# Kernel tuning notes

Measured on AMD Instinct MI355X. Metric: run time of the kernel, lower is better.

Reference implementation:

```python
import math
import jax, jax.numpy as jnp
import numpy as np

H_CYCLES, L_CYCLES = 3, 2
STD = 0.02


def setup_inputs() -> dict:
    key = jax.random.key(0)
    ks = jax.random.split(key, 11)
    D, nh, mult, V, T, B = 512, 8, 64, 8192, 512, 4
    N = mult * D // nh
    def nrm(k, shape):
        return jax.random.normal(k, shape, jnp.float32) * STD
    return {
        "idx": jax.random.randint(ks[0], (B, T), 0, V),
        "embed_w": nrm(ks[1], (V, D)),
        "h_enc": nrm(ks[2], (nh, D, N)),
        "h_enc_v": nrm(ks[3], (nh, D, N)),
        "h_dec": nrm(ks[4], (nh * N, D)),
        "l_enc": nrm(ks[5], (nh, D, N)),
        "l_enc_v": nrm(ks[6], (nh, D, N)),
        "l_dec": nrm(ks[7], (nh * N, D)),
        "lm_head": nrm(ks[8], (D, V)),
        "h_init": nrm(ks[9], (D,)),
        "l_init": nrm(ks[10], (D,)),
    }


def _ln(x, eps=1e-5):
    # LayerNorm without affine params (elementwise_affine=False)
    m = jnp.mean(x, axis=-1, keepdims=True)
    v = jnp.var(x, axis=-1, keepdims=True)
    return (x - m) * jax.lax.rsqrt(v + eps)


def _rope_tables(T, N):
    # freqs with even-quantized exponent, angles wrapped mod 1 then scaled by 2*pi
    q = jnp.floor(jnp.arange(N, dtype=jnp.float32) / 2.0) * 2.0
    freqs = 1.0 / jnp.power(2.0 ** 16, q / N) / (2.0 * math.pi)
    phases = jnp.arange(T, dtype=jnp.float32)[:, None] * freqs[None, :]
    ang = (phases % 1.0) * (2.0 * math.pi)
    return jnp.cos(ang), jnp.sin(ang)  # each (T, N)


def _rope(v, cos, sin):
    # v: (B, nh, T, N); interleaved rotation as in torch stack/view trick
    v_rot = jnp.stack((-v[..., 1::2], v[..., ::2]), axis=-1).reshape(v.shape)
    return v * cos + v_rot * sin


def _attn(x_sparse, Vmat, cos, sin):
    # x_sparse: (B, nh, T, N); Vmat: (B, T, D)
    N = x_sparse.shape[-1]
    T = x_sparse.shape[-2]
    QR = _rope(x_sparse, cos, sin)
    scores = jnp.einsum('bhtn,bhsn->bhts', QR, QR) * (N ** -0.5)
    mask = jnp.tril(jnp.ones((T, T), dtype=bool), k=-1)  # strict lower triangle
    scores = jnp.where(mask, scores, 0.0)
    return jnp.einsum('bhts,bsd->bhtd', scores, Vmat)  # (B, nh, T, D)


def _block(x, inj, enc, enc_v, dec, cos, sin):
    # x, inj: (B, 1, T, D)
    B, _, T, D = x.shape
    nh, _, N = enc.shape
    xi = _ln(x + inj)[:, 0]  # (B, T, D)
    x_sparse = jax.nn.relu(jnp.einsum('btd,hdn->bhtn', xi, enc))
    yKV = _ln(_attn(x_sparse, xi, cos, sin))  # (B, nh, T, D)
    y_sparse = jax.nn.relu(jnp.einsum('bhtd,hdn->bhtn', yKV, enc_v))
    xy = (x_sparse * y_sparse).transpose(0, 2, 1, 3).reshape(B, 1, T, nh * N)
    y = _ln(xy @ dec)  # (B, 1, T, D)
    return _ln(x + y)


def reference(idx, embed_w, h_enc, h_enc_v, h_dec, l_enc, l_enc_v, l_dec,
              lm_head, h_init, l_init):
    B, T = idx.shape
    D = embed_w.shape[1]
    N = l_enc.shape[-1]
    cos, sin = _rope_tables(T, N)
    inp = _ln(embed_w[idx])[:, None]  # (B, 1, T, D)
    z_H = jnp.broadcast_to(h_init, (B, 1, T, D))
    z_L = jnp.broadcast_to(l_init, (B, 1, T, D))
    for h in range(H_CYCLES):
        for l in range(L_CYCLES):
            if not (h == H_CYCLES - 1 and l == L_CYCLES - 1):
                z_L = _block(z_L, z_H + inp, l_enc, l_enc_v, l_dec, cos, sin)
        if h < H_CYCLES - 1:
            z_H = _block(z_H, z_L, h_enc, h_enc_v, h_dec, cos, sin)
    z_L = _block(z_L, z_H + inp, l_enc, l_enc_v, l_dec, cos, sin)
    z_H = _block(z_H, z_L, h_enc, h_enc_v, h_dec, cos, sin)
    logits = z_H[:, 0] @ lm_head  # (B, T, vocab)
    return logits
```

## Files before the change

### kernel.cpp

```cpp
#include <hip/hip_runtime.h>

typedef _Float16 f16;
typedef __attribute__((ext_vector_type(8))) _Float16 f16x8;
typedef __attribute__((ext_vector_type(4))) float f32x4;
typedef __attribute__((ext_vector_type(4))) int i32x4;

#define D_  512
#define NH_ 8
#define NS_ 4096
#define TT_ 512
#define BB_ 4
#define VV_ 8192
#define HN_ 32768
#define BT_ 2048


__device__ __forceinline__ void gl16(const void* g, void* l) {
  __builtin_amdgcn_global_load_lds((const __attribute__((address_space(1))) void*)g,
                                   (__attribute__((address_space(3))) void*)l, 16, 0, 0);
}

__device__ __forceinline__ void gemm_core(const f16* __restrict__ A, const f16* __restrict__ B,
    int lda, int ldb, int nk, char* As, char* Bs, f32x4 acc[4][4]) {
  int tid = threadIdx.x;
  int l = tid & 63, wid = tid >> 6;
  int wm = wid >> 1, wn = wid & 1;
  int row0 = tid >> 3, g0 = tid & 7;
  for (int kt = 0; kt < nk; ++kt) {
    __syncthreads();
#pragma unroll
    for (int it = 0; it < 4; ++it) {
      int row = row0 + 32 * it;
      int gs = g0 ^ (row & 7);
      int wb = (wid * 64 + it * 256) * 16;
      gl16(A + (size_t)row * lda + gs * 8, As + wb);
      gl16(B + (size_t)row * ldb + gs * 8, Bs + wb);
    }
    __syncthreads();
    A += 64; B += 64;
#pragma unroll
    for (int kh = 0; kh < 2; ++kh) {
      f16x8 af[4], bfr[4];
#pragma unroll
      for (int m = 0; m < 4; ++m) {
        int row = wm * 64 + m * 16 + (l & 15);
        af[m] = *(const f16x8*)(As + row * 128 + ((kh * 64 + (l >> 4) * 16) ^ ((row & 7) << 4)));
      }
#pragma unroll
      for (int n = 0; n < 4; ++n) {
        int row = wn * 64 + n * 16 + (l & 15);
        bfr[n] = *(const f16x8*)(Bs + row * 128 + ((kh * 64 + (l >> 4) * 16) ^ ((row & 7) << 4)));
      }
#pragma unroll
      for (int m = 0; m < 4; ++m)
#pragma unroll
        for (int n = 0; n < 4; ++n)
          acc[m][n] = __builtin_amdgcn_mfma_f32_16x16x32_f16(af[m], bfr[n], acc[m][n], 0, 0, 0);
    }
  }
}

__device__ __forceinline__ void gemm_core_w(const f16* __restrict__ A, const f16* __restrict__ B,
    int lda, int ldb, int nk, char* As, char* Bs, f32x4 acc[4][4]) {
  int tid = threadIdx.x;
  int l = tid & 63, wid = tid >> 6;
  int wm = wid >> 2, wn = wid & 3;
  int row0 = tid >> 3, g0 = tid & 7;
  for (int kt = 0; kt < nk; ++kt) {
    __syncthreads();
#pragma unroll
    for (int it = 0; it < 2; ++it) {
      int row = row0 + 64 * it;
      int gs = g0 ^ (row & 7);
      gl16(A + (size_t)row * lda + gs * 8, As + (wid * 64 + it * 512) * 16);
    }
#pragma unroll
    for (int it = 0; it < 4; ++it) {
      int row = row0 + 64 * it;
      int gs = g0 ^ (row & 7);
      gl16(B + (size_t)row * ldb + gs * 8, Bs + (wid * 64 + it * 512) * 16);
    }
    __syncthreads();
    A += 64; B += 64;
#pragma unroll
    for (int kh = 0; kh < 2; ++kh) {
      f16x8 af[4], bfr[4];
#pragma unroll
      for (int m = 0; m < 4; ++m) {
        int row = wm * 64 + m * 16 + (l & 15);
        af[m] = *(const f16x8*)(As + row * 128 + ((kh * 64 + (l >> 4) * 16) ^ ((row & 7) << 4)));
      }
#pragma unroll
      for (int n = 0; n < 4; ++n) {
        int row = wn * 64 + n * 16 + (l & 15);
        bfr[n] = *(const f16x8*)(Bs + row * 128 + ((kh * 64 + (l >> 4) * 16) ^ ((row & 7) << 4)));
      }
#pragma unroll
      for (int m = 0; m < 4; ++m)
#pragma unroll
        for (int n = 0; n < 4; ++n)
          acc[m][n] = __builtin_amdgcn_mfma_f32_16x16x32_f16(af[m], bfr[n], acc[m][n], 0, 0, 0);
    }
  }
}


__global__ __launch_bounds__(512, 4) void k_gemm_xs(
    const f16* __restrict__ xi, const f16* __restrict__ encT,
    const f16* __restrict__ csT, f16* __restrict__ qr) {
  __shared__ char sh[49152];
  int bid = blockIdx.x;
  int h = bid & 7, k = bid >> 3;
  int nt = k >> 4, mt = k & 15;
  const f16* A = xi + (size_t)mt * 128 * D_;
  const f16* B = encT + ((size_t)h * NS_ + nt * 256) * D_;
  f32x4 acc[4][4] = {};
  gemm_core_w(A, B, D_, D_, D_ / 64, sh, sh + 16384, acc);
  int l = threadIdx.x & 63, wid = threadIdx.x >> 6;
  int wm = wid >> 2, wn = wid & 3;
  int r04 = (l >> 4) * 4, c0 = l & 15;
  int b = mt >> 2, tbase = (mt & 3) * 128;
#pragma unroll
  for (int m = 0; m < 4; ++m)
#pragma unroll
    for (int n = 0; n < 4; ++n)
#pragma unroll
      for (int r = 0; r < 4; ++r) {
        int row = wm * 64 + m * 16 + r04 + r;
        int col = wn * 64 + n * 16 + c0;
        int t = tbase + row;
        int nn = nt * 256 + col;
        float xsv = fmaxf(acc[m][n][r], 0.f);
        float prt = __shfl_xor(xsv, 1);
        int ci = 2 * (t * NS_ + nn);
        float c = (float)csT[ci], s = (float)csT[ci + 1];
        float qv = xsv * c + ((nn & 1) ? prt : -prt) * s;
        size_t o = (((size_t)b * NH_ + h) * TT_ + t) * NS_ + nn;
        qr[o] = (f16)qv;
      }
}

__global__ __launch_bounds__(256, 4) void k_gemm_scores(
    const f16* __restrict__ qr, f16* __restrict__ scores) {
  __shared__ i32x4 As4[1024], Bs4[1024];
  int bid = blockIdx.x;
  int swz = (bid & 7) * 40 + (bid >> 3);
  int x = swz % 10, z = swz / 10;
  int mt = (x >= 6) ? 3 : (x >= 3) ? 2 : (x >= 1) ? 1 : 0;
  int nt = x - mt * (mt + 1) / 2;
  const f16* base = qr + (size_t)z * TT_ * NS_;
  const f16* A = base + (size_t)mt * 128 * NS_;
  const f16* B = base + (size_t)nt * 128 * NS_;
  f32x4 acc[4][4] = {};
  gemm_core(A, B, NS_, NS_, NS_ / 64, (char*)As4, (char*)Bs4, acc);
  int l = threadIdx.x & 63, wid = threadIdx.x >> 6;
  int wm = wid >> 1, wn = wid & 1;
  int r04 = (l >> 4) * 4, c0 = l & 15;
  f16* outp = scores + (size_t)z * TT_ * TT_;
#pragma unroll
  for (int m = 0; m < 4; ++m)
#pragma unroll
    for (int n = 0; n < 4; ++n)
#pragma unroll
      for (int r = 0; r < 4; ++r) {
        int t = mt * 128 + wm * 64 + m * 16 + r04 + r;
        int s_ = nt * 128 + wn * 64 + n * 16 + c0;
        float v = (t > s_) ? acc[m][n][r] * 0.015625f : 0.f;
        outp[(size_t)t * TT_ + s_] = (f16)v;
      }
}

__global__ __launch_bounds__(256, 4) void k_gemm_attn(
    const f16* __restrict__ scores, const f16* __restrict__ xiT, f16* __restrict__ attn) {
  __shared__ i32x4 As4[1024], Bs4[1024];
  int bid = blockIdx.x;
  int swz = (bid & 7) * 64 + (bid >> 3);
  int mt = swz & 3, ntd = (swz >> 2) & 3, z = swz >> 4;
  int b = z >> 3;
  const f16* A = scores + (size_t)z * TT_ * TT_ + (size_t)mt * 128 * TT_;
  const f16* B = xiT + (size_t)b * D_ * TT_ + (size_t)ntd * 128 * TT_;
  f32x4 acc[4][4] = {};
  gemm_core(A, B, TT_, TT_, 2 * mt + 2, (char*)As4, (char*)Bs4, acc);
  int l = threadIdx.x & 63, wid = threadIdx.x >> 6;
  int wm = wid >> 1, wn = wid & 1;
  int r04 = (l >> 4) * 4, c0 = l & 15;
#pragma unroll
  for (int m = 0; m < 4; ++m)
#pragma unroll
    for (int n = 0; n < 4; ++n)
#pragma unroll
      for (int r = 0; r < 4; ++r) {
        int t = mt * 128 + wm * 64 + m * 16 + r04 + r;
        int d = ntd * 128 + wn * 64 + n * 16 + c0;
        attn[((size_t)z * TT_ + t) * D_ + d] = (f16)acc[m][n][r];
      }
}

__global__ __launch_bounds__(512, 4) void k_gemm_xy(
    const f16* __restrict__ ykv, const f16* __restrict__ encvT,
    const f16* __restrict__ csT, f16* __restrict__ qrxy) {
  __shared__ char sh[49152];
  int bid = blockIdx.x;
  int h = bid & 7, k = bid >> 3;
  int b = k >> 6, nt = (k >> 2) & 15, mt = k & 3;
  int z = b * NH_ + h;
  const f16* A = ykv + (size_t)z * TT_ * D_ + (size_t)mt * 128 * D_;
  const f16* B = encvT + ((size_t)h * NS_ + nt * 256) * D_;
  f32x4 acc[4][4] = {};
  gemm_core_w(A, B, D_, D_, D_ / 64, sh, sh + 16384, acc);
  int l = threadIdx.x & 63, wid = threadIdx.x >> 6;
  int wm = wid >> 2, wn = wid & 3;
  int r04 = (l >> 4) * 4, c0 = l & 15;
#pragma unroll
  for (int m = 0; m < 4; ++m)
#pragma unroll
    for (int n = 0; n < 4; ++n)
#pragma unroll
      for (int r = 0; r < 4; ++r) {
        int t = mt * 128 + wm * 64 + m * 16 + r04 + r;
        int nn = nt * 256 + wn * 64 + n * 16 + c0;
        float ys = fmaxf(acc[m][n][r], 0.f);
        size_t o = ((size_t)z * TT_ + t) * NS_ + nn;
        float qv = (float)qrxy[o];
        float prt = __shfl_xor(qv, 1);
        int ci = 2 * (t * NS_ + nn);
        float c = (float)csT[ci], s = (float)csT[ci + 1];
        float xsv = (nn & 1) ? (qv * c - prt * s) : (qv * c + prt * s);
        qrxy[o] = (f16)(xsv * ys);
      }
}

__global__ __launch_bounds__(512, 4) void k_gemm_ydec(
    const f16* __restrict__ xy, const f16* __restrict__ decT, f16* __restrict__ ypart) {
  __shared__ char sh[49152];
  int bid = blockIdx.x;
  int kz = bid & 7, k = bid >> 3;
  int mt = k >> 1, nt = k & 1;
  int b = mt >> 2, t0 = (mt & 3) * 128;
  const f16* A = xy + ((size_t)(b * NH_ + kz) * TT_ + t0) * NS_;
  const f16* B = decT + (size_t)nt * 256 * HN_ + (size_t)kz * NS_;
  f32x4 acc[4][4] = {};
  gemm_core_w(A, B, NS_, HN_, NS_ / 64, sh, sh + 16384, acc);
  int l = threadIdx.x & 63, wid = threadIdx.x >> 6;
  int wm = wid >> 2, wn = wid & 3;
  int r04 = (l >> 4) * 4, c0 = l & 15;
  f16* outp = ypart + (size_t)kz * BT_ * D_;
#pragma unroll
  for (int m = 0; m < 4; ++m)
#pragma unroll
    for (int n = 0; n < 4; ++n)
#pragma unroll
      for (int r = 0; r < 4; ++r) {
        int R = mt * 128 + wm * 64 + m * 16 + r04 + r;
        int c = nt * 256 + wn * 64 + n * 16 + c0;
        outp[(size_t)R * D_ + c] = (f16)acc[m][n][r];
      }
}

__global__ __launch_bounds__(512, 4) void k_gemm_logits(
    const f16* __restrict__ zbf, const f16* __restrict__ lmT, float* __restrict__ outp) {
  __shared__ char sh[49152];
  int bid = blockIdx.x;
  int xcd = bid & 7, k = bid >> 3;
  int nt = xcd * 4 + (k >> 4), mt = k & 15;
  const f16* A = zbf + (size_t)mt * 128 * D_;
  const f16* B = lmT + (size_t)nt * 256 * D_;
  f32x4 acc[4][4] = {};
  gemm_core_w(A, B, D_, D_, D_ / 64, sh, sh + 16384, acc);
  int l = threadIdx.x & 63, wid = threadIdx.x >> 6;
  int wm = wid >> 2, wn = wid & 3;
  int r04 = (l >> 4) * 4, c0 = l & 15;
#pragma unroll
  for (int m = 0; m < 4; ++m)
#pragma unroll
    for (int n = 0; n < 4; ++n)
#pragma unroll
      for (int r = 0; r < 4; ++r) {
        int R = mt * 128 + wm * 64 + m * 16 + r04 + r;
        int v = nt * 256 + wn * 64 + n * 16 + c0;
        outp[(size_t)R * VV_ + v] = acc[m][n][r];
      }
}


__device__ __forceinline__ float wave_sum(float v) {
#pragma unroll
  for (int o = 32; o > 0; o >>= 1) v += __shfl_xor(v, o);
  return v;
}

__global__ __launch_bounds__(256) void k_tables(f16* __restrict__ csT) {
  int i = blockIdx.x * 256 + threadIdx.x;
  int t = i >> 12, n = i & (NS_ - 1);
  float q = (float)(n & ~1);
  float freq = exp2f(-16.f * q / 4096.f) * 0.15915494309189535f;
  float ph = (float)t * freq;
  ph -= floorf(ph);
  float ang = ph * 6.283185307179586f;
  csT[2 * i]     = (f16)cosf(ang);
  csT[2 * i + 1] = (f16)sinf(ang);
}

__global__ void k_transpose(const float* __restrict__ in, f16* __restrict__ outp, int R, int C) {
  __shared__ float tile[32][33];
  size_t mo = (size_t)blockIdx.z * R * C;
  in += mo; outp += mo;
  int c0 = blockIdx.x * 32, r0 = blockIdx.y * 32;
#pragma unroll
  for (int i = threadIdx.y; i < 32; i += 8)
    tile[i][threadIdx.x] = in[(size_t)(r0 + i) * C + c0 + threadIdx.x];
  __syncthreads();
#pragma unroll
  for (int i = threadIdx.y; i < 32; i += 8)
    outp[(size_t)(c0 + i) * R + r0 + threadIdx.x] = (f16)tile[threadIdx.x][i];
}

__global__ __launch_bounds__(256) void k_embed_ln(const int* __restrict__ idx,
    const float* __restrict__ emb, f16* __restrict__ inp) {
  int r = blockIdx.x * 4 + (threadIdx.x >> 6);
  int lane = threadIdx.x & 63;
  const float* e = emb + (size_t)idx[r] * D_ + lane * 8;
  f32x4 e0 = *(const f32x4*)e;
  f32x4 e1 = *(const f32x4*)(e + 4);
  float v[8];
#pragma unroll
  for (int i = 0; i < 4; ++i) { v[i] = e0[i]; v[i + 4] = e1[i]; }
  float s = 0.f;
#pragma unroll
  for (int i = 0; i < 8; ++i) s += v[i];
  float mean = wave_sum(s) * (1.f / 512.f);
  float q = 0.f;
#pragma unroll
  for (int i = 0; i < 8; ++i) { v[i] -= mean; q += v[i] * v[i]; }
  float rs = rsqrtf(wave_sum(q) * (1.f / 512.f) + 1e-5f);
  f16x8 ov;
#pragma unroll
  for (int i = 0; i < 8; ++i) ov[i] = (f16)(v[i] * rs);
  *(f16x8*)(inp + (size_t)r * D_ + lane * 8) = ov;
}

__global__ __launch_bounds__(256) void k_init(const float* __restrict__ hi,
    const float* __restrict__ li, f16* __restrict__ zH, f16* __restrict__ zL) {
  size_t i = (size_t)blockIdx.x * 256 + threadIdx.x;
  zH[i] = (f16)hi[i & (D_ - 1)];
  zL[i] = (f16)li[i & (D_ - 1)];
}

__global__ __launch_bounds__(256) void k_ln_xi(const f16* __restrict__ x,
    const f16* __restrict__ a1, const f16* __restrict__ a2,
    f16* __restrict__ xi, f16* __restrict__ xiT) {
  int r = blockIdx.x * 4 + (threadIdx.x >> 6);
  int lane = threadIdx.x & 63;
  size_t o = (size_t)r * D_ + lane * 8;
  f16x8 xv = *(const f16x8*)(x + o);
  f16x8 av = *(const f16x8*)(a1 + o);
  float v[8];
#pragma unroll
  for (int i = 0; i < 8; ++i) v[i] = (float)xv[i] + (float)av[i];
  if (a2) {
    f16x8 bv = *(const f16x8*)(a2 + o);
#pragma unroll
    for (int i = 0; i < 8; ++i) v[i] += (float)bv[i];
  }
  float s = 0.f;
#pragma unroll
  for (int i = 0; i < 8; ++i) s += v[i];
  float mean = wave_sum(s) * (1.f / 512.f);
  float q = 0.f;
#pragma unroll
  for (int i = 0; i < 8; ++i) { v[i] -= mean; q += v[i] * v[i]; }
  float rs = rsqrtf(wave_sum(q) * (1.f / 512.f) + 1e-5f);
  f16x8 ov;
#pragma unroll
  for (int i = 0; i < 8; ++i) ov[i] = (f16)(v[i] * rs);
  *(f16x8*)(xi + o) = ov;
  int b = r >> 9, t = r & (TT_ - 1);
  int d0 = lane * 8;
#pragma unroll
  for (int i = 0; i < 8; ++i)
    xiT[((size_t)b * D_ + d0 + i) * TT_ + t] = ov[i];
}

__global__ __launch_bounds__(256) void k_ln_rows(const f16* __restrict__ in, f16* __restrict__ outp) {
  int r = blockIdx.x * 4 + (threadIdx.x >> 6);
  int lane = threadIdx.x & 63;
  size_t o = (size_t)r * D_ + lane * 8;
  f16x8 xv = *(const f16x8*)(in + o);
  float v[8];
#pragma unroll
  for (int i = 0; i < 8; ++i) v[i] = (float)xv[i];
  float s = 0.f;
#pragma unroll
  for (int i = 0; i < 8; ++i) s += v[i];
  float mean = wave_sum(s) * (1.f / 512.f);
  float q = 0.f;
#pragma unroll
  for (int i = 0; i < 8; ++i) { v[i] -= mean; q += v[i] * v[i]; }
  float rs = rsqrtf(wave_sum(q) * (1.f / 512.f) + 1e-5f);
  f16x8 ov;
#pragma unroll
  for (int i = 0; i < 8; ++i) ov[i] = (f16)(v[i] * rs);
  *(f16x8*)(outp + o) = ov;
}

__global__ __launch_bounds__(256) void k_ln_y_out(const f16* __restrict__ ypart,
    f16* __restrict__ z) {
  int r = blockIdx.x * 4 + (threadIdx.x >> 6);
  int lane = threadIdx.x & 63;
  size_t o = (size_t)r * D_ + lane * 8;
  float v[8] = {};
#pragma unroll
  for (int k = 0; k < 8; ++k) {
    f16x8 p = *(const f16x8*)(ypart + (size_t)k * BT_ * D_ + o);
#pragma unroll
    for (int i = 0; i < 8; ++i) v[i] += (float)p[i];
  }
  float s = 0.f;
#pragma unroll
  for (int i = 0; i < 8; ++i) s += v[i];
  float mean = wave_sum(s) * (1.f / 512.f);
  float q = 0.f;
#pragma unroll
  for (int i = 0; i < 8; ++i) { v[i] -= mean; q += v[i] * v[i]; }
  float rs = rsqrtf(wave_sum(q) * (1.f / 512.f) + 1e-5f);
  f16x8 zv = *(const f16x8*)(z + o);
#pragma unroll
  for (int i = 0; i < 8; ++i) v[i] = (float)zv[i] + v[i] * rs;
  s = 0.f;
#pragma unroll
  for (int i = 0; i < 8; ++i) s += v[i];
  mean = wave_sum(s) * (1.f / 512.f);
  q = 0.f;
#pragma unroll
  for (int i = 0; i < 8; ++i) { v[i] -= mean; q += v[i] * v[i]; }
  rs = rsqrtf(wave_sum(q) * (1.f / 512.f) + 1e-5f);
  f16x8 ov;
#pragma unroll
  for (int i = 0; i < 8; ++i) ov[i] = (f16)(v[i] * rs);
  *(f16x8*)(z + o) = ov;
}


extern "C" void kernel_launch(void* const* d_in, const int* in_sizes, int n_in,
                              void* d_out, int out_size, void* d_ws, size_t ws_size,
                              hipStream_t stream) {
  (void)in_sizes; (void)n_in; (void)out_size;
  const int*   idx    = (const int*)  d_in[0];
  const float* emb    = (const float*)d_in[1];
  const float* h_enc  = (const float*)d_in[2];
  const float* h_encv = (const float*)d_in[3];
  const float* h_dec  = (const float*)d_in[4];
  const float* l_enc  = (const float*)d_in[5];
  const float* l_encv = (const float*)d_in[6];
  const float* l_dec  = (const float*)d_in[7];
  const float* lm     = (const float*)d_in[8];
  const float* h_init = (const float*)d_in[9];
  const float* l_init = (const float*)d_in[10];
  float* out = (float*)d_out;

  bool resident = ws_size >= ((size_t)352 << 20);

  char* w = (char*)d_ws;
  size_t off = 0;
  auto alloc = [&](size_t n) { void* p = w + off; off += (n + 255) & ~(size_t)255; return p; };
  f16* csT = (f16*)alloc(8388608);
  f16 *encT[2], *encvT[2], *decT[2], *lmT;
  if (resident) {
    for (int s = 0; s < 2; ++s) {
      encT[s]  = (f16*)alloc(33554432);
      encvT[s] = (f16*)alloc(33554432);
      decT[s]  = (f16*)alloc(33554432);
    }
    lmT = (f16*)alloc(8388608);
  } else {
    encT[0]  = encT[1]  = (f16*)alloc(33554432);
    encvT[0] = encvT[1] = (f16*)alloc(33554432);
    decT[0]  = decT[1]  = (f16*)alloc(33554432);
    lmT = encT[0];
  }
  f16* inp    = (f16*)alloc(2097152);
  f16* zH     = (f16*)alloc(2097152);
  f16* zL     = (f16*)alloc(2097152);
  f16* xi_bf  = (f16*)alloc(2097152);
  f16* xiT_bf = (f16*)alloc(2097152);
  f16* qrxy   = (f16*)alloc(134217728);

  f16* scoresB = (f16*)d_out;
  f16* attnP   = (f16*)((char*)d_out + 16777216);
  f16* ypart   = attnP;
  f16* ykv     = (f16*)((char*)d_out + 33554432);

  dim3 tb(32, 8);
  auto transpose_set = [&](int sel) {
    const float* e  = sel ? h_enc  : l_enc;
    const float* ev = sel ? h_encv : l_encv;
    const float* dc = sel ? h_dec  : l_dec;
    k_transpose<<<dim3(128, 16, 8), tb, 0, stream>>>(e,  encT[sel],  512, 4096);
    k_transpose<<<dim3(128, 16, 8), tb, 0, stream>>>(ev, encvT[sel], 512, 4096);
    k_transpose<<<dim3(16, 1024, 1), tb, 0, stream>>>(dc, decT[sel], 32768, 512);
  };

  k_tables<<<8192, 256, 0, stream>>>(csT);
  k_embed_ln<<<512, 256, 0, stream>>>(idx, emb, inp);
  k_init<<<4096, 256, 0, stream>>>(h_init, l_init, zH, zL);
  if (resident) {
    transpose_set(0);
    transpose_set(1);
    k_transpose<<<dim3(256, 16, 1), tb, 0, stream>>>(lm, lmT, 512, 8192);
  }

  int cur = -1;
  auto setw = [&](int sel) {
    if (resident || cur == sel) { cur = sel; return; }
    cur = sel;
    transpose_set(sel);
  };

  auto run_block = [&](f16* zx, const f16* a1, const f16* a2, int s) {
    k_ln_xi<<<512, 256, 0, stream>>>(zx, a1, a2, xi_bf, xiT_bf);
    k_gemm_xs<<<2048, 512, 0, stream>>>(xi_bf, encT[s], csT, qrxy);
    k_gemm_scores<<<320, 256, 0, stream>>>(qrxy, scoresB);
    k_gemm_attn<<<512, 256, 0, stream>>>(scoresB, xiT_bf, attnP);
    k_ln_rows<<<4096, 256, 0, stream>>>(attnP, ykv);
    k_gemm_xy<<<2048, 512, 0, stream>>>(ykv, encvT[s], csT, qrxy);
    k_gemm_ydec<<<256, 512, 0, stream>>>(qrxy, decT[s], ypart);
    k_ln_y_out<<<512, 256, 0, stream>>>(ypart, zx);
  };

  for (int i = 0; i < 3; ++i) {
    setw(0);
    run_block(zL, inp, zH, 0);
    run_block(zL, inp, zH, 0);
    setw(1);
    run_block(zH, zL, (const f16*)nullptr, 1);
  }
  if (!resident)
    k_transpose<<<dim3(256, 16, 1), tb, 0, stream>>>(lm, lmT, 512, 8192);
  k_gemm_logits<<<512, 512, 0, stream>>>(zH, lmT, out);
}
```

Measured before the change: 4.375 ms.

## Retile GEMM kernels: 256x256 tiles for xs/xy, 128x128 for ydec/logits

The xs and xy GEMMs move to a new core that computes a 256x256 tile per 512-thread block. Each wave now holds 8x4 MFMA accumulators, which raises operand reuse and halves the block count. The ydec and logits GEMMs switch to the 128x128, 256-thread core so more blocks run in parallel. The rope cos/sin pair is now read with one vector load. The larger tiles raise register and LDS use, which lowers occupancy, and launch bounds are cut to 2 blocks per CU.

```diff
diff --git a/kernel.cpp b/kernel.cpp
--- a/kernel.cpp
+++ b/kernel.cpp
@@ -1,6 +1,7 @@
 #include <hip/hip_runtime.h>
 
 typedef _Float16 f16;
+typedef __attribute__((ext_vector_type(2))) _Float16 f16x2;
 typedef __attribute__((ext_vector_type(8))) _Float16 f16x8;
 typedef __attribute__((ext_vector_type(4))) float f32x4;
 typedef __attribute__((ext_vector_type(4))) int i32x4;
@@ -60,8 +61,8 @@
   }
 }
 
-__device__ __forceinline__ void gemm_core_w(const f16* __restrict__ A, const f16* __restrict__ B,
-    int lda, int ldb, int nk, char* As, char* Bs, f32x4 acc[4][4]) {
+__device__ __forceinline__ void gemm_core2(const f16* __restrict__ A, const f16* __restrict__ B,
+    int lda, int ldb, int nk, char* As, char* Bs, f32x4 acc[8][4]) {
   int tid = threadIdx.x;
   int l = tid & 63, wid = tid >> 6;
   int wm = wid >> 2, wn = wid & 3;
@@ -69,25 +70,21 @@
   for (int kt = 0; kt < nk; ++kt) {
     __syncthreads();
 #pragma unroll
-    for (int it = 0; it < 2; ++it) {
-      int row = row0 + 64 * it;
-      int gs = g0 ^ (row & 7);
-      gl16(A + (size_t)row * lda + gs * 8, As + (wid * 64 + it * 512) * 16);
-    }
-#pragma unroll
     for (int it = 0; it < 4; ++it) {
       int row = row0 + 64 * it;
       int gs = g0 ^ (row & 7);
-      gl16(B + (size_t)row * ldb + gs * 8, Bs + (wid * 64 + it * 512) * 16);
+      int wb = (wid * 64 + it * 512) * 16;
+      gl16(A + (size_t)row * lda + gs * 8, As + wb);
+      gl16(B + (size_t)row * ldb + gs * 8, Bs + wb);
     }
     __syncthreads();
     A += 64; B += 64;
 #pragma unroll
     for (int kh = 0; kh < 2; ++kh) {
-      f16x8 af[4], bfr[4];
-#pragma unroll
-      for (int m = 0; m < 4; ++m) {
-        int row = wm * 64 + m * 16 + (l & 15);
+      f16x8 af[8], bfr[4];
+#pragma unroll
+      for (int m = 0; m < 8; ++m) {
+        int row = wm * 128 + m * 16 + (l & 15);
         af[m] = *(const f16x8*)(As + row * 128 + ((kh * 64 + (l >> 4) * 16) ^ ((row & 7) << 4)));
       }
 #pragma unroll
@@ -96,7 +93,7 @@
         bfr[n] = *(const f16x8*)(Bs + row * 128 + ((kh * 64 + (l >> 4) * 16) ^ ((row & 7) << 4)));
       }
 #pragma unroll
-      for (int m = 0; m < 4; ++m)
+      for (int m = 0; m < 8; ++m)
 #pragma unroll
         for (int n = 0; n < 4; ++n)
           acc[m][n] = __builtin_amdgcn_mfma_f32_16x16x32_f16(af[m], bfr[n], acc[m][n], 0, 0, 0);
@@ -105,35 +102,34 @@
 }
 
 
-__global__ __launch_bounds__(512, 4) void k_gemm_xs(
+__global__ __launch_bounds__(512, 2) void k_gemm_xs(
     const f16* __restrict__ xi, const f16* __restrict__ encT,
     const f16* __restrict__ csT, f16* __restrict__ qr) {
-  __shared__ char sh[49152];
+  __shared__ char sh[65536];
   int bid = blockIdx.x;
   int h = bid & 7, k = bid >> 3;
-  int nt = k >> 4, mt = k & 15;
-  const f16* A = xi + (size_t)mt * 128 * D_;
+  int nt = k >> 3, mt = k & 7;
+  const f16* A = xi + (size_t)mt * 256 * D_;
   const f16* B = encT + ((size_t)h * NS_ + nt * 256) * D_;
-  f32x4 acc[4][4] = {};
-  gemm_core_w(A, B, D_, D_, D_ / 64, sh, sh + 16384, acc);
+  f32x4 acc[8][4] = {};
+  gemm_core2(A, B, D_, D_, D_ / 64, sh, sh + 32768, acc);
   int l = threadIdx.x & 63, wid = threadIdx.x >> 6;
   int wm = wid >> 2, wn = wid & 3;
   int r04 = (l >> 4) * 4, c0 = l & 15;
-  int b = mt >> 2, tbase = (mt & 3) * 128;
-#pragma unroll
-  for (int m = 0; m < 4; ++m)
+#pragma unroll
+  for (int m = 0; m < 8; ++m)
 #pragma unroll
     for (int n = 0; n < 4; ++n)
 #pragma unroll
       for (int r = 0; r < 4; ++r) {
-        int row = wm * 64 + m * 16 + r04 + r;
-        int col = wn * 64 + n * 16 + c0;
-        int t = tbase + row;
-        int nn = nt * 256 + col;
+        int row = wm * 128 + m * 16 + r04 + r;
+        int R = mt * 256 + row;
+        int b = R >> 9, t = R & (TT_ - 1);
+        int nn = nt * 256 + wn * 64 + n * 16 + c0;
         float xsv = fmaxf(acc[m][n][r], 0.f);
         float prt = __shfl_xor(xsv, 1);
-        int ci = 2 * (t * NS_ + nn);
-        float c = (float)csT[ci], s = (float)csT[ci + 1];
+        f16x2 cs = *(const f16x2*)(csT + 2 * ((size_t)t * NS_ + nn));
+        float c = (float)cs[0], s = (float)cs[1];
         float qv = xsv * c + ((nn & 1) ? prt : -prt) * s;
         size_t o = (((size_t)b * NH_ + h) * TT_ + t) * NS_ + nn;
         qr[o] = (f16)qv;
@@ -196,53 +192,53 @@
       }
 }
 
-__global__ __launch_bounds__(512, 4) void k_gemm_xy(
+__global__ __launch_bounds__(512, 2) void k_gemm_xy(
     const f16* __restrict__ ykv, const f16* __restrict__ encvT,
     const f16* __restrict__ csT, f16* __restrict__ qrxy) {
-  __shared__ char sh[49152];
+  __shared__ char sh[65536];
   int bid = blockIdx.x;
   int h = bid & 7, k = bid >> 3;
-  int b = k >> 6, nt = (k >> 2) & 15, mt = k & 3;
+  int b = k >> 5, nt = (k >> 1) & 15, mt = k & 1;
   int z = b * NH_ + h;
-  const f16* A = ykv + (size_t)z * TT_ * D_ + (size_t)mt * 128 * D_;
+  const f16* A = ykv + ((size_t)z * TT_ + mt * 256) * D_;
   const f16* B = encvT + ((size_t)h * NS_ + nt * 256) * D_;
-  f32x4 acc[4][4] = {};
-  gemm_core_w(A, B, D_, D_, D_ / 64, sh, sh + 16384, acc);
+  f32x4 acc[8][4] = {};
+  gemm_core2(A, B, D_, D_, D_ / 64, sh, sh + 32768, acc);
   int l = threadIdx.x & 63, wid = threadIdx.x >> 6;
   int wm = wid >> 2, wn = wid & 3;
   int r04 = (l >> 4) * 4, c0 = l & 15;
 #pragma unroll
-  for (int m = 0; m < 4; ++m)
+  for (int m = 0; m < 8; ++m)
 #pragma unroll
     for (int n = 0; n < 4; ++n)
 #pragma unroll
       for (int r = 0; r < 4; ++r) {
-        int t = mt * 128 + wm * 64 + m * 16 + r04 + r;
+        int t = mt * 256 + wm * 128 + m * 16 + r04 + r;
         int nn = nt * 256 + wn * 64 + n * 16 + c0;
         float ys = fmaxf(acc[m][n][r], 0.f);
         size_t o = ((size_t)z * TT_ + t) * NS_ + nn;
         float qv = (float)qrxy[o];
         float prt = __shfl_xor(qv, 1);
-        int ci = 2 * (t * NS_ + nn);
-        float c = (float)csT[ci], s = (float)csT[ci + 1];
+        f16x2 cs = *(const f16x2*)(csT + 2 * ((size_t)t * NS_ + nn));
+        float c = (float)cs[0], s = (float)cs[1];
         float xsv = (nn & 1) ? (qv * c - prt * s) : (qv * c + prt * s);
         qrxy[o] = (f16)(xsv * ys);
       }
 }
 
-__global__ __launch_bounds__(512, 4) void k_gemm_ydec(
+__global__ __launch_bounds__(256, 4) void k_gemm_ydec(
     const f16* __restrict__ xy, const f16* __restrict__ decT, f16* __restrict__ ypart) {
-  __shared__ char sh[49152];
+  __shared__ i32x4 As4[1024], Bs4[1024];
   int bid = blockIdx.x;
-  int kz = bid & 7, k = bid >> 3;
-  int mt = k >> 1, nt = k & 1;
+  int xcd = bid & 7, k = bid >> 3;
+  int kz = xcd, mt = k >> 2, nt = k & 3;
   int b = mt >> 2, t0 = (mt & 3) * 128;
   const f16* A = xy + ((size_t)(b * NH_ + kz) * TT_ + t0) * NS_;
-  const f16* B = decT + (size_t)nt * 256 * HN_ + (size_t)kz * NS_;
+  const f16* B = decT + (size_t)nt * 128 * HN_ + (size_t)kz * NS_;
   f32x4 acc[4][4] = {};
-  gemm_core_w(A, B, NS_, HN_, NS_ / 64, sh, sh + 16384, acc);
+  gemm_core(A, B, NS_, HN_, NS_ / 64, (char*)As4, (char*)Bs4, acc);
   int l = threadIdx.x & 63, wid = threadIdx.x >> 6;
-  int wm = wid >> 2, wn = wid & 3;
+  int wm = wid >> 1, wn = wid & 1;
   int r04 = (l >> 4) * 4, c0 = l & 15;
   f16* outp = ypart + (size_t)kz * BT_ * D_;
 #pragma unroll
@@ -252,23 +248,23 @@
 #pragma unroll
       for (int r = 0; r < 4; ++r) {
         int R = mt * 128 + wm * 64 + m * 16 + r04 + r;
-        int c = nt * 256 + wn * 64 + n * 16 + c0;
+        int c = nt * 128 + wn * 64 + n * 16 + c0;
         outp[(size_t)R * D_ + c] = (f16)acc[m][n][r];
       }
 }
 
-__global__ __launch_bounds__(512, 4) void k_gemm_logits(
+__global__ __launch_bounds__(256, 4) void k_gemm_logits(
     const f16* __restrict__ zbf, const f16* __restrict__ lmT, float* __restrict__ outp) {
-  __shared__ char sh[49152];
+  __shared__ i32x4 As4[1024], Bs4[1024];
   int bid = blockIdx.x;
   int xcd = bid & 7, k = bid >> 3;
-  int nt = xcd * 4 + (k >> 4), mt = k & 15;
+  int nt = xcd * 8 + (k >> 4), mt = k & 15;
   const f16* A = zbf + (size_t)mt * 128 * D_;
-  const f16* B = lmT + (size_t)nt * 256 * D_;
+  const f16* B = lmT + (size_t)nt * 128 * D_;
   f32x4 acc[4][4] = {};
-  gemm_core_w(A, B, D_, D_, D_ / 64, sh, sh + 16384, acc);
+  gemm_core(A, B, D_, D_, D_ / 64, (char*)As4, (char*)Bs4, acc);
   int l = threadIdx.x & 63, wid = threadIdx.x >> 6;
-  int wm = wid >> 2, wn = wid & 3;
+  int wm = wid >> 1, wn = wid & 1;
   int r04 = (l >> 4) * 4, c0 = l & 15;
 #pragma unroll
   for (int m = 0; m < 4; ++m)
@@ -277,7 +273,7 @@
 #pragma unroll
       for (int r = 0; r < 4; ++r) {
         int R = mt * 128 + wm * 64 + m * 16 + r04 + r;
-        int v = nt * 256 + wn * 64 + n * 16 + c0;
+        int v = nt * 128 + wn * 64 + n * 16 + c0;
         outp[(size_t)R * VV_ + v] = acc[m][n][r];
       }
 }
@@ -518,12 +514,12 @@
 
   auto run_block = [&](f16* zx, const f16* a1, const f16* a2, int s) {
     k_ln_xi<<<512, 256, 0, stream>>>(zx, a1, a2, xi_bf, xiT_bf);
-    k_gemm_xs<<<2048, 512, 0, stream>>>(xi_bf, encT[s], csT, qrxy);
+    k_gemm_xs<<<1024, 512, 0, stream>>>(xi_bf, encT[s], csT, qrxy);
     k_gemm_scores<<<320, 256, 0, stream>>>(qrxy, scoresB);
     k_gemm_attn<<<512, 256, 0, stream>>>(scoresB, xiT_bf, attnP);
     k_ln_rows<<<4096, 256, 0, stream>>>(attnP, ykv);
-    k_gemm_xy<<<2048, 512, 0, stream>>>(ykv, encvT[s], csT, qrxy);
-    k_gemm_ydec<<<256, 512, 0, stream>>>(qrxy, decT[s], ypart);
+    k_gemm_xy<<<1024, 512, 0, stream>>>(ykv, encvT[s], csT, qrxy);
+    k_gemm_ydec<<<512, 256, 0, stream>>>(qrxy, decT[s], ypart);
     k_ln_y_out<<<512, 256, 0, stream>>>(ypart, zx);
   };
 
@@ -536,5 +532,5 @@
   }
   if (!resident)
     k_transpose<<<dim3(256, 16, 1), tb, 0, stream>>>(lm, lmT, 512, 8192);
-  k_gemm_logits<<<512, 512, 0, stream>>>(zH, lmT, out);
-}
+  k_gemm_logits<<<1024, 256, 0, stream>>>(zH, lmT, out);
+}
```

New measurement: 4.425 ms. No clear change (+1.1%).
